# Optimization experiments

Measured on AMD Instinct MI355X. Metric: run time of the kernel, lower is better.

Reference implementation:

```python
import jax, jax.numpy as jnp
import numpy as np

D_IN = 1024
D_OUT = 1024


def setup_inputs() -> dict:
    key = jax.random.key(0)
    kx, kq, kk, kv = jax.random.split(key, 4)
    B, S = 4, 2048
    scale = 1.0 / np.sqrt(D_IN)
    return {
        "x": jax.random.normal(kx, (B, S, D_IN), dtype=jnp.float32),
        "Wq": jax.random.normal(kq, (D_IN, D_OUT), dtype=jnp.float32) * scale,
        "Wk": jax.random.normal(kk, (D_IN, D_OUT), dtype=jnp.float32) * scale,
        "Wv": jax.random.normal(kv, (D_IN, D_OUT), dtype=jnp.float32) * scale,
    }


def reference(x, Wq, Wk, Wv):
    # x: [B, S, D_in]; single-head causal attention (dropout=0 -> identity)
    q = jnp.einsum("bsd,de->bse", x, Wq)
    k = jnp.einsum("bsd,de->bse", x, Wk)
    v = jnp.einsum("bsd,de->bse", x, Wv)
    S = x.shape[1]
    d_k = k.shape[-1]
    scores = jnp.einsum("bqe,bke->bqk", q, k) / jnp.sqrt(jnp.float32(d_k))
    causal = jnp.tril(jnp.ones((S, S), dtype=bool))  # True = keep
    scores = jnp.where(causal, scores, -jnp.inf)
    weights = jax.nn.softmax(scores, axis=-1)
    return jnp.einsum("bqk,bke->bqe", weights, v)
```

## Files before the change

### kernel.cpp

```cpp
#include <hip/hip_runtime.h>

typedef unsigned short u16;
typedef __bf16 bf16x8_v __attribute__((ext_vector_type(8)));
typedef float f32x4 __attribute__((ext_vector_type(4)));

__device__ __forceinline__ u16 f2bf(float f) {
    unsigned u = __float_as_uint(f);
    unsigned r = u + 0x7fffu + ((u >> 16) & 1u);
    return (u16)(r >> 16);
}
__device__ __forceinline__ float bf2f(u16 h) {
    return __uint_as_float(((unsigned)h) << 16);
}

__device__ __forceinline__ void gll16(const u16* g, u16* l) {
    __builtin_amdgcn_global_load_lds(
        (const __attribute__((address_space(1))) void*)g,
        (__attribute__((address_space(3))) void*)l, 16, 0, 0);
}

#define EXP_SHIFT 12.0f

__device__ __forceinline__ float* srow_ptr(u16* Sb, int b, int i) {
    return (float*)((char*)Sb + (size_t)b * 8388608 +
                    ((i >> 9) << 12) + 2048 + ((size_t)(i & 511) << 2));
}

__global__ __launch_bounds__(256) void k_prep(const float* __restrict__ x,
                                              const float* __restrict__ Wq,
                                              const float* __restrict__ Wk,
                                              const float* __restrict__ Wv,
                                              u16* __restrict__ xb,
                                              u16* __restrict__ Wt3,
                                              u16* __restrict__ Sb) {
    __shared__ float tile[32][33];
    const int bid = blockIdx.x, tid = threadIdx.x;
    if (bid < 4096) {
        int i = (bid * 256 + tid) * 8;
        float4 a = *(const float4*)(x + i);
        float4 bb = *(const float4*)(x + i + 4);
        union { int4 p; u16 h[8]; } o;
        o.h[0] = f2bf(a.x);  o.h[1] = f2bf(a.y);  o.h[2] = f2bf(a.z);  o.h[3] = f2bf(a.w);
        o.h[4] = f2bf(bb.x); o.h[5] = f2bf(bb.y); o.h[6] = f2bf(bb.z); o.h[7] = f2bf(bb.w);
        *(int4*)(xb + i) = o.p;
    } else if (bid < 7168) {
        const int w = bid - 4096;
        const int z = w >> 10, rem = w & 1023;
        const int bx = rem & 31, by = rem >> 5;
        const float* W = (z == 0) ? Wq : (z == 1) ? Wk : Wv;
        u16* Wt = Wt3 + (size_t)z * 1024 * 1024;
        const int tx = tid & 31, ty = tid >> 5;
#pragma unroll
        for (int r = 0; r < 4; ++r)
            tile[ty + r * 8][tx] = W[(by * 32 + ty + r * 8) * 1024 + bx * 32 + tx];
        __syncthreads();
#pragma unroll
        for (int r = 0; r < 4; ++r)
            Wt[(bx * 32 + ty + r * 8) * 1024 + by * 32 + tx] =
                f2bf(tile[tx][ty + r * 8]);
    } else {
        const int chunk = tid >> 7;
        const int t = tid & 127;
#pragma unroll
        for (int c = 0; c < 8; ++c) {
            const int cc = c * 2 + chunk;
            char* p = (char*)Sb + (size_t)(cc >> 2) * 8388608 +
                      ((cc & 3) << 12) + 2048;
            int4 z4 = {0, 0, 0, 0};
            *(int4*)(p + t * 16) = z4;
        }
    }
}

__device__ __forceinline__ void gemm_core_nt(const u16* __restrict__ A,
                                             const u16* __restrict__ B,
                                             int lda, int ldb, int kLen,
                                             u16* smem, f32x4 acc[4][4]) {
    u16* As = smem;
    u16* Bs = smem + 128 * 64;
    const int tid = threadIdx.x;
    const int wave = tid >> 6;
    const int lane = tid & 63;
    const int rowA = tid >> 3;
    const int kcs  = (tid & 7) ^ (rowA & 7);
    const int row16 = lane & 15;
    const int quad = lane >> 4;
    const int sw = row16 & 7;
    const int wm = (wave >> 1) * 64;
    const int wn = (wave & 1) * 64;

#pragma unroll
    for (int i = 0; i < 4; ++i)
#pragma unroll
        for (int j = 0; j < 4; ++j) {
            f32x4 z = {0.f, 0.f, 0.f, 0.f};
            acc[i][j] = z;
        }

    const u16* Ag[4]; const u16* Bg[4];
    u16 *AsB[4], *BsB[4];
#pragma unroll
    for (int u = 0; u < 4; ++u) {
        Ag[u] = A + (size_t)(u * 32 + rowA) * lda + kcs * 8;
        Bg[u] = B + (size_t)(u * 32 + rowA) * ldb + kcs * 8;
        AsB[u] = As + (u * 256 + wave * 64) * 8;
        BsB[u] = Bs + (u * 256 + wave * 64) * 8;
    }

    const int ktiles = kLen >> 6;
    for (int kt = 0; kt < ktiles; ++kt) {
        __syncthreads();
#pragma unroll
        for (int u = 0; u < 4; ++u) gll16(Ag[u] + kt * 64, AsB[u]);
#pragma unroll
        for (int u = 0; u < 4; ++u) gll16(Bg[u] + kt * 64, BsB[u]);
        __syncthreads();
#pragma unroll
        for (int h = 0; h < 2; ++h) {
            bf16x8_v af[4], bfv[4];
            const int cp = (h * 4 + quad);
#pragma unroll
            for (int i = 0; i < 4; ++i)
                af[i] = *(const bf16x8_v*)(As + (wm + i * 16 + row16) * 64 +
                                           (cp ^ sw) * 8);
#pragma unroll
            for (int j = 0; j < 4; ++j)
                bfv[j] = *(const bf16x8_v*)(Bs + (wn + j * 16 + row16) * 64 +
                                            (cp ^ sw) * 8);
#pragma unroll
            for (int i = 0; i < 4; ++i)
#pragma unroll
                for (int j = 0; j < 4; ++j)
                    acc[i][j] = __builtin_amdgcn_mfma_f32_16x16x32_bf16(
                        af[i], bfv[j], acc[i][j], 0, 0, 0);
        }
    }
}

__device__ __forceinline__ void epi_bf16(const f32x4 acc[4][4], u16* smem,
                                         u16* __restrict__ g, int ldg) {
    const int tid = threadIdx.x;
    const int wave = tid >> 6, lane = tid & 63;
    const int row16 = lane & 15, quad = lane >> 4;
    u16* Ts = smem + wave * 2048;
#pragma unroll
    for (int jh = 0; jh < 2; ++jh) {
#pragma unroll
        for (int i = 0; i < 4; ++i)
#pragma unroll
            for (int jj = 0; jj < 2; ++jj) {
                const int j = jh * 2 + jj;
#pragma unroll
                for (int r = 0; r < 4; ++r)
                    Ts[(i * 16 + quad * 4 + r) * 32 + jj * 16 + row16] =
                        f2bf(acc[i][j][r]);
            }
#pragma unroll
        for (int s = 0; s < 4; ++s) {
            const int row = s * 16 + (lane >> 2);
            int4 val = *(const int4*)(Ts + row * 32 + (lane & 3) * 8);
            *(int4*)(g + (size_t)row * ldg + jh * 32 + (lane & 3) * 8) = val;
        }
    }
}

__device__ __forceinline__ void epi_vt(const f32x4 acc[4][4], u16* smem,
                                       u16* __restrict__ Vt, int m0w, int n0w) {
    const int tid = threadIdx.x;
    const int wave = tid >> 6, lane = tid & 63;
    const int row16 = lane & 15, quad = lane >> 4;
    const int b = m0w >> 11;
    const int sBase = m0w & 2047;
    u16* Ts = smem + wave * 4608;
#pragma unroll
    for (int p = 0; p < 2; ++p) {
#pragma unroll
        for (int i = 0; i < 4; ++i)
#pragma unroll
            for (int jj = 0; jj < 2; ++jj) {
                const int j = p * 2 + jj;
                union { unsigned long long d; u16 h[4]; } o;
#pragma unroll
                for (int r = 0; r < 4; ++r) o.h[r] = f2bf(acc[i][j][r]);
                *(unsigned long long*)(Ts + (jj * 16 + row16) * 72 +
                                       i * 16 + quad * 4) = o.d;
            }
#pragma unroll
        for (int rr = 0; rr < 4; ++rr) {
            const int ln = rr * 8 + (lane >> 3);
            const int ck = lane & 7;
            int4 val = *(const int4*)(Ts + ln * 72 + ck * 8);
            const int n = n0w + p * 32 + ln;
            *(int4*)(Vt + ((size_t)b * 1024 + n) * 2048 + sBase + ck * 8) = val;
        }
    }
}

__global__ __launch_bounds__(256, 3) void k_gemm_proj(const u16* __restrict__ X,
                                                      const u16* __restrict__ Wt3,
                                                      u16* __restrict__ Qb,
                                                      u16* __restrict__ Kb,
                                                      u16* __restrict__ Vt) {
    __shared__ u16 smem[18432];
    const int n0g = blockIdx.x * 128, m0 = blockIdx.y * 128;
    f32x4 acc[4][4];
    gemm_core_nt(X + (size_t)m0 * 1024, Wt3 + (size_t)n0g * 1024, 1024, 1024, 1024,
                 smem, acc);
    const int tid = threadIdx.x, wave = tid >> 6;
    const int wm = (wave >> 1) * 64, wn = (wave & 1) * 64;
    __syncthreads();
    if (n0g < 2048) {
        u16* Y = (n0g < 1024) ? Qb : Kb;
        const int n0 = n0g & 1023;
        epi_bf16(acc, smem, Y + (size_t)(m0 + wm) * 1024 + n0 + wn, 1024);
    } else {
        epi_vt(acc, smem, Vt, m0 + wm, (n0g - 2048) + wn);
    }
}

__global__ __launch_bounds__(256, 4) void k_gemm_scores(const u16* __restrict__ Q,
                                                        const u16* __restrict__ Kb,
                                                        u16* __restrict__ Sb) {
    __shared__ u16 smem[16384];
    int t = blockIdx.x, b = blockIdx.y;
    int mt = 0;
    while ((mt + 1) * (mt + 2) / 2 <= t) ++mt;
    int nt = t - mt * (mt + 1) / 2;
    const u16* Qp = Q + (size_t)b * 2048 * 1024 + (size_t)mt * 128 * 1024;
    const u16* Kp = Kb + (size_t)b * 2048 * 1024 + (size_t)nt * 128 * 1024;
    u16* Sp = Sb + (size_t)b * 2048 * 2048;
    f32x4 acc[4][4];
    gemm_core_nt(Qp, Kp, 1024, 1024, 1024, smem, acc);
    const int tid = threadIdx.x, wave = tid >> 6, lane = tid & 63;
    const int wm = (wave >> 1) * 64, wn = (wave & 1) * 64;
    const int row16 = lane & 15, quad = lane >> 4;
    const int mBase = mt * 128 + wm;
    const int nBase = nt * 128 + wn;
    u16* Ts = smem + wave * 2048;
    float rs[4][4];
#pragma unroll
    for (int i = 0; i < 4; ++i)
#pragma unroll
        for (int r = 0; r < 4; ++r) rs[i][r] = 0.f;

    __syncthreads();
#pragma unroll
    for (int jh = 0; jh < 2; ++jh) {
#pragma unroll
        for (int i = 0; i < 4; ++i)
#pragma unroll
            for (int jj = 0; jj < 2; ++jj) {
                const int j = jh * 2 + jj;
                const int n = nBase + jh * 32 + jj * 16 + row16;
#pragma unroll
                for (int r = 0; r < 4; ++r) {
                    const int m = mBase + i * 16 + quad * 4 + r;
                    float e = 0.f;
                    if (n <= m)
                        e = __expf(acc[i][j][r] * 0.03125f - EXP_SHIFT);
                    rs[i][r] += e;
                    Ts[(i * 16 + quad * 4 + r) * 32 + jj * 16 + row16] = f2bf(e);
                }
            }
#pragma unroll
        for (int s = 0; s < 4; ++s) {
            const int row = s * 16 + (lane >> 2);
            int4 val = *(const int4*)(Ts + row * 32 + (lane & 3) * 8);
            *(int4*)(Sp + (size_t)(mBase + row) * 2048 +
                     nBase + jh * 32 + (lane & 3) * 8) = val;
        }
    }
#pragma unroll
    for (int i = 0; i < 4; ++i)
#pragma unroll
        for (int r = 0; r < 4; ++r) {
            float s = rs[i][r];
#pragma unroll
            for (int off = 1; off < 16; off <<= 1) s += __shfl_xor(s, off);
            if (row16 == 0)
                atomicAdd(srow_ptr((u16*)Sb, b, mBase + i * 16 + quad * 4 + r), s);
        }
}

__global__ __launch_bounds__(256, 4) void k_gemm_pv(u16* __restrict__ P,
                                                    const u16* __restrict__ Vt,
                                                    float* __restrict__ O) {
    __shared__ u16 smem[16384];
    const int nt = blockIdx.x, mt = 15 - blockIdx.y, b = blockIdx.z;
    const u16* Pp = P + (size_t)b * 2048 * 2048 + (size_t)mt * 128 * 2048;
    const u16* Vp = Vt + (size_t)b * 1024 * 2048 + (size_t)nt * 128 * 2048;
    f32x4 acc[4][4];
    gemm_core_nt(Pp, Vp, 2048, 2048, (mt + 1) * 128, smem, acc);
    float* Op = O + (size_t)b * 2048 * 1024;
    const int tid = threadIdx.x, wave = tid >> 6, lane = tid & 63;
    const int wm = (wave >> 1) * 64, wn = (wave & 1) * 64;
    const int row16 = lane & 15, quad = lane >> 4;
    float inv[4][4];
#pragma unroll
    for (int i = 0; i < 4; ++i)
#pragma unroll
        for (int r = 0; r < 4; ++r)
            inv[i][r] = 1.0f / *srow_ptr(P, b, mt * 128 + wm + i * 16 + quad * 4 + r);
#pragma unroll
    for (int i = 0; i < 4; ++i)
#pragma unroll
        for (int j = 0; j < 4; ++j) {
            int m = mt * 128 + wm + i * 16 + quad * 4;
            int n = nt * 128 + wn + j * 16 + row16;
#pragma unroll
            for (int r = 0; r < 4; ++r)
                Op[(size_t)(m + r) * 1024 + n] = acc[i][j][r] * inv[i][r];
        }
}

extern "C" void kernel_launch(void* const* d_in, const int* in_sizes, int n_in,
                              void* d_out, int out_size, void* d_ws, size_t ws_size,
                              hipStream_t stream) {
    const float* x  = (const float*)d_in[0];
    const float* Wq = (const float*)d_in[1];
    const float* Wk = (const float*)d_in[2];
    const float* Wv = (const float*)d_in[3];
    float* out = (float*)d_out;
    char* ws = (char*)d_ws;

    u16* xb  = (u16*)(ws);
    u16* Wt3 = (u16*)(ws + (16u << 20));
    u16* Qb  = (u16*)(ws + (22u << 20));
    u16* Kb  = (u16*)(ws + (38u << 20));
    u16* Vt  = (u16*)(ws + (54u << 20));
    u16* Sb  = (u16*)(ws + (70u << 20));

    k_prep<<<7169, 256, 0, stream>>>(x, Wq, Wk, Wv, xb, Wt3, Sb);
    k_gemm_proj<<<dim3(24, 64), 256, 0, stream>>>(xb, Wt3, Qb, Kb, Vt);
    k_gemm_scores<<<dim3(136, 4), 256, 0, stream>>>(Qb, Kb, Sb);
    k_gemm_pv<<<dim3(8, 16, 4), 256, 0, stream>>>(Sb, Vt, out);
}
```

Before: 232.0 us.

## Rewrite projection GEMM with 256x256 tiles, 4-stage async LDS pipeline

```diff
diff --git a/kernel.cpp b/kernel.cpp
--- a/kernel.cpp
+++ b/kernel.cpp
@@ -196,25 +196,112 @@
     }
 }
 
-__global__ __launch_bounds__(256, 3) void k_gemm_proj(const u16* __restrict__ X,
-                                                      const u16* __restrict__ Wt3,
-                                                      u16* __restrict__ Qb,
-                                                      u16* __restrict__ Kb,
-                                                      u16* __restrict__ Vt) {
-    __shared__ u16 smem[18432];
-    const int n0g = blockIdx.x * 128, m0 = blockIdx.y * 128;
-    f32x4 acc[4][4];
-    gemm_core_nt(X + (size_t)m0 * 1024, Wt3 + (size_t)n0g * 1024, 1024, 1024, 1024,
-                 smem, acc);
-    const int tid = threadIdx.x, wave = tid >> 6;
-    const int wm = (wave >> 1) * 64, wn = (wave & 1) * 64;
-    __syncthreads();
+__global__ __launch_bounds__(512, 2) void k_gemm_proj2(
+    const u16* __restrict__ X, const u16* __restrict__ Wt3,
+    u16* __restrict__ Qb, u16* __restrict__ Kb, u16* __restrict__ Vt) {
+    extern __shared__ u16 lds[];
+    const int tid = threadIdx.x;
+    const int wave = tid >> 6, lane = tid & 63;
+    const int row16 = lane & 15, quad = lane >> 4;
+
+    const int bid = blockIdx.x;
+    const int lin = (bid & 7) * 48 + (bid >> 3);
+    const int mt = lin / 12, nt = lin - mt * 12;
+    const int m0 = mt << 8, n0g = nt << 8;
+
+    const u16* Ag = X + (size_t)m0 * 1024;
+    const u16* Bg = Wt3 + (size_t)n0g * 1024;
+
+    const int r0 = wave * 32 + (lane >> 2);
+    const int r1 = r0 + 16;
+    const int c0 = (lane & 3) ^ ((r0 >> 1) & 3);
+    const int c1 = (lane & 3) ^ ((r1 >> 1) & 3);
+    const u16* gA0 = Ag + (size_t)r0 * 1024 + c0 * 8;
+    const u16* gA1 = Ag + (size_t)r1 * 1024 + c1 * 8;
+    const u16* gB0 = Bg + (size_t)r0 * 1024 + c0 * 8;
+    const u16* gB1 = Bg + (size_t)r1 * 1024 + c1 * 8;
+    u16* ldsA0 = lds + (wave * 2 + 0) * 512;
+    u16* ldsA1 = lds + (wave * 2 + 1) * 512;
+    u16* ldsB0 = ldsA0 + 8192;
+    u16* ldsB1 = ldsA1 + 8192;
+
+#define STAGE_A(t_) do { const int b_ = ((t_) & 3) * 16384, k_ = (t_) * 32; \
+        gll16(gA0 + k_, ldsA0 + b_); gll16(gA1 + k_, ldsA1 + b_); } while (0)
+#define STAGE_B(t_) do { const int b_ = ((t_) & 3) * 16384, k_ = (t_) * 32; \
+        gll16(gB0 + k_, ldsB0 + b_); gll16(gB1 + k_, ldsB1 + b_); } while (0)
+
+    const int wm = (wave >> 2) * 128, wn = (wave & 3) * 64;
+    const int sw8 = (quad ^ ((row16 >> 1) & 3)) << 3;
+    int offA[8], offB[4];
+#pragma unroll
+    for (int i = 0; i < 8; ++i) offA[i] = (wm + i * 16 + row16) * 32 + sw8;
+#pragma unroll
+    for (int j = 0; j < 4; ++j) offB[j] = (wn + j * 16 + row16) * 32 + sw8 + 8192;
+
+    f32x4 acc[8][4];
+#pragma unroll
+    for (int i = 0; i < 8; ++i)
+#pragma unroll
+        for (int j = 0; j < 4; ++j) { f32x4 z = {0.f, 0.f, 0.f, 0.f}; acc[i][j] = z; }
+
+    const int ktiles = 32;
+    STAGE_A(0); STAGE_B(0);
+    STAGE_A(1); STAGE_B(1);
+    STAGE_A(2); STAGE_B(2);
+
+    for (int t = 0; t < ktiles; ++t) {
+        if (t <= ktiles - 3)
+            asm volatile("s_waitcnt vmcnt(8)" ::: "memory");
+        else if (t == ktiles - 2)
+            asm volatile("s_waitcnt vmcnt(4)" ::: "memory");
+        else
+            asm volatile("s_waitcnt vmcnt(0)" ::: "memory");
+        asm volatile("s_barrier" ::: "memory");
+
+        const u16* buf = lds + (t & 3) * 16384;
+        bf16x8_v bq[4], aq[4];
+#pragma unroll
+        for (int j = 0; j < 4; ++j) bq[j] = *(const bf16x8_v*)(buf + offB[j]);
+#pragma unroll
+        for (int i = 0; i < 4; ++i) aq[i] = *(const bf16x8_v*)(buf + offA[i]);
+        if (t + 3 < ktiles) STAGE_A(t + 3);
+        __builtin_amdgcn_s_setprio(1);
+#pragma unroll
+        for (int i = 0; i < 4; ++i)
+#pragma unroll
+            for (int j = 0; j < 4; ++j)
+                acc[i][j] = __builtin_amdgcn_mfma_f32_16x16x32_bf16(
+                    aq[i], bq[j], acc[i][j], 0, 0, 0);
+        __builtin_amdgcn_s_setprio(0);
+#pragma unroll
+        for (int i = 0; i < 4; ++i) aq[i] = *(const bf16x8_v*)(buf + offA[4 + i]);
+        if (t + 3 < ktiles) STAGE_B(t + 3);
+        __builtin_amdgcn_s_setprio(1);
+#pragma unroll
+        for (int i = 0; i < 4; ++i)
+#pragma unroll
+            for (int j = 0; j < 4; ++j)
+                acc[4 + i][j] = __builtin_amdgcn_mfma_f32_16x16x32_bf16(
+                    aq[i], bq[j], acc[4 + i][j], 0, 0, 0);
+        __builtin_amdgcn_s_setprio(0);
+    }
+#undef STAGE_A
+#undef STAGE_B
+
+    asm volatile("s_waitcnt lgkmcnt(0)" ::: "memory");
+    asm volatile("s_barrier" ::: "memory");
+
     if (n0g < 2048) {
         u16* Y = (n0g < 1024) ? Qb : Kb;
         const int n0 = n0g & 1023;
-        epi_bf16(acc, smem, Y + (size_t)(m0 + wm) * 1024 + n0 + wn, 1024);
+#pragma unroll
+        for (int hf = 0; hf < 2; ++hf)
+            epi_bf16(acc + hf * 4, lds,
+                     Y + (size_t)(m0 + wm + hf * 64) * 1024 + n0 + wn, 1024);
     } else {
-        epi_vt(acc, smem, Vt, m0 + wm, (n0g - 2048) + wn);
+#pragma unroll
+        for (int hf = 0; hf < 2; ++hf)
+            epi_vt(acc + hf * 4, lds, Vt, m0 + wm + hf * 64, (n0g - 2048) + wn);
     }
 }
 
@@ -330,8 +417,15 @@
     u16* Vt  = (u16*)(ws + (54u << 20));
     u16* Sb  = (u16*)(ws + (70u << 20));
 
+    static bool s_attr_done = false;
+    if (!s_attr_done) {
+        hipFuncSetAttribute(reinterpret_cast<const void*>(k_gemm_proj2),
+                            hipFuncAttributeMaxDynamicSharedMemorySize, 131072);
+        s_attr_done = true;
+    }
+
     k_prep<<<7169, 256, 0, stream>>>(x, Wq, Wk, Wv, xb, Wt3, Sb);
-    k_gemm_proj<<<dim3(24, 64), 256, 0, stream>>>(xb, Wt3, Qb, Kb, Vt);
+    k_gemm_proj2<<<dim3(384), dim3(512), 131072, stream>>>(xb, Wt3, Qb, Kb, Vt);
     k_gemm_scores<<<dim3(136, 4), 256, 0, stream>>>(Qb, Kb, Sb);
     k_gemm_pv<<<dim3(8, 16, 4), 256, 0, stream>>>(Sb, Vt, out);
 }
```

After: 236.7 us. 2.0% more time.

## Rewrite QKV projection GEMM as 256x256 ping-pong pipelined kernel with 8 waves

Applied to the files above, without the earlier changes.

```diff
diff --git a/kernel.cpp b/kernel.cpp
--- a/kernel.cpp
+++ b/kernel.cpp
@@ -196,25 +196,134 @@
     }
 }
 
-__global__ __launch_bounds__(256, 3) void k_gemm_proj(const u16* __restrict__ X,
-                                                      const u16* __restrict__ Wt3,
-                                                      u16* __restrict__ Qb,
-                                                      u16* __restrict__ Kb,
-                                                      u16* __restrict__ Vt) {
-    __shared__ u16 smem[18432];
-    const int n0g = blockIdx.x * 128, m0 = blockIdx.y * 128;
-    f32x4 acc[4][4];
-    gemm_core_nt(X + (size_t)m0 * 1024, Wt3 + (size_t)n0g * 1024, 1024, 1024, 1024,
-                 smem, acc);
-    const int tid = threadIdx.x, wave = tid >> 6;
-    const int wm = (wave >> 1) * 64, wn = (wave & 1) * 64;
-    __syncthreads();
+#define BAR  asm volatile("s_barrier" ::: "memory")
+#define VMW4 asm volatile("s_waitcnt vmcnt(4)" ::: "memory")
+#define VMW0 asm volatile("s_waitcnt vmcnt(0)" ::: "memory")
+#define STAGE(LB, GP, KT, H) do { \
+    gll16((GP) + (size_t)((H) * 128) * 1024 + (KT) * 64, \
+          (LB) + ((H) * 128) * 64 + wave * 512); \
+    gll16((GP) + (size_t)((H) * 128 + 64) * 1024 + (KT) * 64, \
+          (LB) + ((H) * 128 + 64) * 64 + wave * 512); } while (0)
+#define LDA_LO(BUF) do { _Pragma("unroll") for (int i = 0; i < 4; ++i) { \
+    a0[i] = *(const bf16x8_v*)((BUF) + offA[i]); \
+    a1[i] = *(const bf16x8_v*)((BUF) + (offA[i] ^ 32)); } } while (0)
+#define LDA_HI(BUF) do { _Pragma("unroll") for (int i = 0; i < 4; ++i) { \
+    a0[i] = *(const bf16x8_v*)((BUF) + offA[4 + i]); \
+    a1[i] = *(const bf16x8_v*)((BUF) + (offA[4 + i] ^ 32)); } } while (0)
+#define LDB_K0(BUF) do { _Pragma("unroll") for (int j = 0; j < 4; ++j) \
+    b0[j] = *(const bf16x8_v*)((BUF) + offB[j]); } while (0)
+#define LDB_K1(BUF) do { _Pragma("unroll") for (int j = 0; j < 4; ++j) \
+    b1[j] = *(const bf16x8_v*)((BUF) + (offB[j] ^ 32)); } while (0)
+#define MFMA16(IOFF, AA, BB) do { __builtin_amdgcn_s_setprio(1); \
+    _Pragma("unroll") for (int i = 0; i < 4; ++i) \
+    _Pragma("unroll") for (int j = 0; j < 4; ++j) \
+        acc[(IOFF) + i][j] = __builtin_amdgcn_mfma_f32_16x16x32_bf16( \
+            AA[i], BB[j], acc[(IOFF) + i][j], 0, 0, 0); \
+    __builtin_amdgcn_s_setprio(0); } while (0)
+
+__global__ __launch_bounds__(512, 2) void k_gemm_proj2(
+    const u16* __restrict__ X, const u16* __restrict__ Wt3,
+    u16* __restrict__ Qb, u16* __restrict__ Kb, u16* __restrict__ Vt) {
+    extern __shared__ u16 lds[];
+    const int tid = threadIdx.x;
+    const int wave = tid >> 6, lane = tid & 63;
+    const int row16 = lane & 15, quad = lane >> 4;
+
+    const int bid = blockIdx.x;
+    const int lin = (bid & 7) * 48 + (bid >> 3);
+    const int mt = lin / 12, nt = lin - mt * 12;
+    const int m0 = mt << 8, n0g = nt << 8;
+
+    const int rowls = wave * 8 + (lane >> 3);
+    const int chk = ((lane & 7) ^ ((lane >> 3) & 7)) << 3;
+    const u16* gA = X + (size_t)(m0 + rowls) * 1024 + chk;
+    const u16* gB = Wt3 + (size_t)(n0g + rowls) * 1024 + chk;
+
+    u16* A0b = lds;
+    u16* B0b = lds + 16384;
+    u16* A1b = lds + 32768;
+    u16* B1b = lds + 49152;
+
+    const int wm = (wave >> 2) * 128, wn = (wave & 3) * 64;
+    const int csw = (quad ^ (row16 & 7)) << 3;
+    int offA[8], offB[4];
+#pragma unroll
+    for (int i = 0; i < 8; ++i) offA[i] = (wm + i * 16 + row16) * 64 + csw;
+#pragma unroll
+    for (int j = 0; j < 4; ++j) offB[j] = (wn + j * 16 + row16) * 64 + csw;
+
+    f32x4 acc[8][4];
+#pragma unroll
+    for (int i = 0; i < 8; ++i)
+#pragma unroll
+        for (int j = 0; j < 4; ++j) { f32x4 z = {0.f, 0.f, 0.f, 0.f}; acc[i][j] = z; }
+
+    STAGE(A0b, gA, 0, 0); STAGE(A0b, gA, 0, 1);
+    STAGE(B0b, gB, 0, 0); STAGE(B0b, gB, 0, 1);
+    STAGE(B1b, gB, 1, 0); STAGE(B1b, gB, 1, 1);
+    VMW4; BAR;
+
+    bf16x8_v a0[4], a1[4], b0[4], b1[4];
+
+    for (int I = 0; I < 7; ++I) {
+        const int kt1 = 2 * I + 1, ktA = 2 * I + 2, ktB = 2 * I + 3;
+        LDA_LO(A0b); LDB_K0(B0b);
+        STAGE(A1b, gA, kt1, 0);
+        BAR; MFMA16(0, a0, b0); BAR;
+        LDB_K1(B0b);
+        STAGE(A1b, gA, kt1, 1);
+        BAR; MFMA16(0, a1, b1); BAR;
+        LDA_HI(A0b);
+        STAGE(B0b, gB, ktA, 0);
+        BAR; MFMA16(4, a0, b0); BAR;
+        STAGE(B0b, gB, ktA, 1);
+        VMW4;
+        BAR; MFMA16(4, a1, b1); BAR;
+        LDA_LO(A1b); LDB_K0(B1b);
+        STAGE(A0b, gA, ktA, 0);
+        BAR; MFMA16(0, a0, b0); BAR;
+        LDB_K1(B1b);
+        STAGE(A0b, gA, ktA, 1);
+        BAR; MFMA16(0, a1, b1); BAR;
+        LDA_HI(A1b);
+        STAGE(B1b, gB, ktB, 0);
+        BAR; MFMA16(4, a0, b0); BAR;
+        STAGE(B1b, gB, ktB, 1);
+        VMW4;
+        BAR; MFMA16(4, a1, b1); BAR;
+    }
+    {
+        LDA_LO(A0b); LDB_K0(B0b);
+        STAGE(A1b, gA, 15, 0);
+        BAR; MFMA16(0, a0, b0); BAR;
+        LDB_K1(B0b);
+        STAGE(A1b, gA, 15, 1);
+        BAR; MFMA16(0, a1, b1); BAR;
+        LDA_HI(A0b);
+        BAR; MFMA16(4, a0, b0); BAR;
+        VMW0;
+        BAR; MFMA16(4, a1, b1); BAR;
+        LDA_LO(A1b); LDB_K0(B1b);
+        BAR; MFMA16(0, a0, b0); BAR;
+        LDB_K1(B1b);
+        BAR; MFMA16(0, a1, b1); BAR;
+        LDA_HI(A1b);
+        BAR; MFMA16(4, a0, b0); BAR;
+        MFMA16(4, a1, b1);
+        BAR;
+    }
+
     if (n0g < 2048) {
         u16* Y = (n0g < 1024) ? Qb : Kb;
         const int n0 = n0g & 1023;
-        epi_bf16(acc, smem, Y + (size_t)(m0 + wm) * 1024 + n0 + wn, 1024);
+#pragma unroll
+        for (int hf = 0; hf < 2; ++hf)
+            epi_bf16(acc + hf * 4, lds,
+                     Y + (size_t)(m0 + wm + hf * 64) * 1024 + n0 + wn, 1024);
     } else {
-        epi_vt(acc, smem, Vt, m0 + wm, (n0g - 2048) + wn);
+#pragma unroll
+        for (int hf = 0; hf < 2; ++hf)
+            epi_vt(acc + hf * 4, lds, Vt, m0 + wm + hf * 64, (n0g - 2048) + wn);
     }
 }
 
@@ -330,8 +439,15 @@
     u16* Vt  = (u16*)(ws + (54u << 20));
     u16* Sb  = (u16*)(ws + (70u << 20));
 
+    static bool s_attr_done = false;
+    if (!s_attr_done) {
+        hipFuncSetAttribute(reinterpret_cast<const void*>(k_gemm_proj2),
+                            hipFuncAttributeMaxDynamicSharedMemorySize, 131072);
+        s_attr_done = true;
+    }
+
     k_prep<<<7169, 256, 0, stream>>>(x, Wq, Wk, Wv, xb, Wt3, Sb);
-    k_gemm_proj<<<dim3(24, 64), 256, 0, stream>>>(xb, Wt3, Qb, Kb, Vt);
+    k_gemm_proj2<<<dim3(384), dim3(512), 131072, stream>>>(xb, Wt3, Qb, Kb, Vt);
     k_gemm_scores<<<dim3(136, 4), 256, 0, stream>>>(Qb, Kb, Sb);
     k_gemm_pv<<<dim3(8, 16, 4), 256, 0, stream>>>(Sb, Vt, out);
 }
```

New measurement: 234.9 us. About the same (+1.3%).

## Fuse scores and PV kernels into persistent kernel with dependency counters

Applied to the files above, without the earlier changes.

```diff
diff --git a/kernel.cpp b/kernel.cpp
--- a/kernel.cpp
+++ b/kernel.cpp
@@ -61,14 +61,16 @@
     } else {
         const int chunk = tid >> 7;
         const int t = tid & 127;
+        int4 z4 = {0, 0, 0, 0};
 #pragma unroll
         for (int c = 0; c < 8; ++c) {
             const int cc = c * 2 + chunk;
             char* p = (char*)Sb + (size_t)(cc >> 2) * 8388608 +
                       ((cc & 3) << 12) + 2048;
-            int4 z4 = {0, 0, 0, 0};
             *(int4*)(p + t * 16) = z4;
         }
+        if (tid < 64)
+            *(int4*)((char*)Sb + 1024 + tid * 16) = z4;
     }
 }
 
@@ -218,99 +220,128 @@
     }
 }
 
-__global__ __launch_bounds__(256, 4) void k_gemm_scores(const u16* __restrict__ Q,
-                                                        const u16* __restrict__ Kb,
-                                                        u16* __restrict__ Sb) {
+__global__ __launch_bounds__(256, 4) void k_sp(const u16* __restrict__ Q,
+                                               const u16* __restrict__ Kb,
+                                               u16* __restrict__ Sb,
+                                               const u16* __restrict__ Vt,
+                                               float* __restrict__ O) {
     __shared__ u16 smem[16384];
-    int t = blockIdx.x, b = blockIdx.y;
-    int mt = 0;
-    while ((mt + 1) * (mt + 2) / 2 <= t) ++mt;
-    int nt = t - mt * (mt + 1) / 2;
-    const u16* Qp = Q + (size_t)b * 2048 * 1024 + (size_t)mt * 128 * 1024;
-    const u16* Kp = Kb + (size_t)b * 2048 * 1024 + (size_t)nt * 128 * 1024;
-    u16* Sp = Sb + (size_t)b * 2048 * 2048;
-    f32x4 acc[4][4];
-    gemm_core_nt(Qp, Kp, 1024, 1024, 1024, smem, acc);
+    __shared__ int s_id;
+    int* ctr = (int*)((char*)Sb + 1024);
     const int tid = threadIdx.x, wave = tid >> 6, lane = tid & 63;
     const int wm = (wave >> 1) * 64, wn = (wave & 1) * 64;
     const int row16 = lane & 15, quad = lane >> 4;
-    const int mBase = mt * 128 + wm;
-    const int nBase = nt * 128 + wn;
-    u16* Ts = smem + wave * 2048;
-    float rs[4][4];
-#pragma unroll
-    for (int i = 0; i < 4; ++i)
-#pragma unroll
-        for (int r = 0; r < 4; ++r) rs[i][r] = 0.f;
-
-    __syncthreads();
-#pragma unroll
-    for (int jh = 0; jh < 2; ++jh) {
-#pragma unroll
-        for (int i = 0; i < 4; ++i)
-#pragma unroll
-            for (int jj = 0; jj < 2; ++jj) {
-                const int j = jh * 2 + jj;
-                const int n = nBase + jh * 32 + jj * 16 + row16;
-#pragma unroll
-                for (int r = 0; r < 4; ++r) {
-                    const int m = mBase + i * 16 + quad * 4 + r;
-                    float e = 0.f;
-                    if (n <= m)
-                        e = __expf(acc[i][j][r] * 0.03125f - EXP_SHIFT);
-                    rs[i][r] += e;
-                    Ts[(i * 16 + quad * 4 + r) * 32 + jj * 16 + row16] = f2bf(e);
+
+    for (;;) {
+        __syncthreads();
+        if (tid == 0)
+            s_id = __hip_atomic_fetch_add(&ctr[0], 1, __ATOMIC_RELAXED,
+                                          __HIP_MEMORY_SCOPE_AGENT);
+        __syncthreads();
+        const int id = s_id;
+        if (id >= 1056) return;
+
+        if (id < 544) {
+            const int b = id / 136;
+            const int t = 135 - (id % 136);
+            int mt = 0;
+            while ((mt + 1) * (mt + 2) / 2 <= t) ++mt;
+            const int nt = t - mt * (mt + 1) / 2;
+            const u16* Qp = Q + (size_t)b * 2048 * 1024 + (size_t)mt * 128 * 1024;
+            const u16* Kp = Kb + (size_t)b * 2048 * 1024 + (size_t)nt * 128 * 1024;
+            u16* Sp = Sb + (size_t)b * 2048 * 2048;
+            f32x4 acc[4][4];
+            gemm_core_nt(Qp, Kp, 1024, 1024, 1024, smem, acc);
+            const int mBase = mt * 128 + wm;
+            const int nBase = nt * 128 + wn;
+            u16* Ts = smem + wave * 2048;
+            float rs[4][4];
+#pragma unroll
+            for (int i = 0; i < 4; ++i)
+#pragma unroll
+                for (int r = 0; r < 4; ++r) rs[i][r] = 0.f;
+
+            __syncthreads();
+#pragma unroll
+            for (int jh = 0; jh < 2; ++jh) {
+#pragma unroll
+                for (int i = 0; i < 4; ++i)
+#pragma unroll
+                    for (int jj = 0; jj < 2; ++jj) {
+                        const int j = jh * 2 + jj;
+                        const int n = nBase + jh * 32 + jj * 16 + row16;
+#pragma unroll
+                        for (int r = 0; r < 4; ++r) {
+                            const int m = mBase + i * 16 + quad * 4 + r;
+                            float e = 0.f;
+                            if (n <= m)
+                                e = __expf(acc[i][j][r] * 0.03125f - EXP_SHIFT);
+                            rs[i][r] += e;
+                            Ts[(i * 16 + quad * 4 + r) * 32 + jj * 16 + row16] =
+                                f2bf(e);
+                        }
+                    }
+#pragma unroll
+                for (int s = 0; s < 4; ++s) {
+                    const int row = s * 16 + (lane >> 2);
+                    int4 val = *(const int4*)(Ts + row * 32 + (lane & 3) * 8);
+                    *(int4*)(Sp + (size_t)(mBase + row) * 2048 +
+                             nBase + jh * 32 + (lane & 3) * 8) = val;
                 }
             }
 #pragma unroll
-        for (int s = 0; s < 4; ++s) {
-            const int row = s * 16 + (lane >> 2);
-            int4 val = *(const int4*)(Ts + row * 32 + (lane & 3) * 8);
-            *(int4*)(Sp + (size_t)(mBase + row) * 2048 +
-                     nBase + jh * 32 + (lane & 3) * 8) = val;
-        }
-    }
-#pragma unroll
-    for (int i = 0; i < 4; ++i)
-#pragma unroll
-        for (int r = 0; r < 4; ++r) {
-            float s = rs[i][r];
-#pragma unroll
-            for (int off = 1; off < 16; off <<= 1) s += __shfl_xor(s, off);
-            if (row16 == 0)
-                atomicAdd(srow_ptr((u16*)Sb, b, mBase + i * 16 + quad * 4 + r), s);
-        }
-}
-
-__global__ __launch_bounds__(256, 4) void k_gemm_pv(u16* __restrict__ P,
-                                                    const u16* __restrict__ Vt,
-                                                    float* __restrict__ O) {
-    __shared__ u16 smem[16384];
-    const int nt = blockIdx.x, mt = 15 - blockIdx.y, b = blockIdx.z;
-    const u16* Pp = P + (size_t)b * 2048 * 2048 + (size_t)mt * 128 * 2048;
-    const u16* Vp = Vt + (size_t)b * 1024 * 2048 + (size_t)nt * 128 * 2048;
-    f32x4 acc[4][4];
-    gemm_core_nt(Pp, Vp, 2048, 2048, (mt + 1) * 128, smem, acc);
-    float* Op = O + (size_t)b * 2048 * 1024;
-    const int tid = threadIdx.x, wave = tid >> 6, lane = tid & 63;
-    const int wm = (wave >> 1) * 64, wn = (wave & 1) * 64;
-    const int row16 = lane & 15, quad = lane >> 4;
-    float inv[4][4];
-#pragma unroll
-    for (int i = 0; i < 4; ++i)
-#pragma unroll
-        for (int r = 0; r < 4; ++r)
-            inv[i][r] = 1.0f / *srow_ptr(P, b, mt * 128 + wm + i * 16 + quad * 4 + r);
-#pragma unroll
-    for (int i = 0; i < 4; ++i)
-#pragma unroll
-        for (int j = 0; j < 4; ++j) {
-            int m = mt * 128 + wm + i * 16 + quad * 4;
-            int n = nt * 128 + wn + j * 16 + row16;
-#pragma unroll
-            for (int r = 0; r < 4; ++r)
-                Op[(size_t)(m + r) * 1024 + n] = acc[i][j][r] * inv[i][r];
-        }
+            for (int i = 0; i < 4; ++i)
+#pragma unroll
+                for (int r = 0; r < 4; ++r) {
+                    float s = rs[i][r];
+#pragma unroll
+                    for (int off = 1; off < 16; off <<= 1) s += __shfl_xor(s, off);
+                    if (row16 == 0)
+                        atomicAdd(srow_ptr(Sb, b, mBase + i * 16 + quad * 4 + r), s);
+                }
+            __threadfence();
+            __syncthreads();
+            if (tid == 0)
+                __hip_atomic_fetch_add(&ctr[2 + b * 16 + mt], 1,
+                                       __ATOMIC_RELEASE,
+                                       __HIP_MEMORY_SCOPE_AGENT);
+        } else {
+            const int p = id - 544;
+            const int mt = 15 - (p >> 5);
+            const int b = (p >> 3) & 3;
+            const int nt = p & 7;
+            if (tid == 0) {
+                while (__hip_atomic_load(&ctr[2 + b * 16 + mt],
+                                         __ATOMIC_RELAXED,
+                                         __HIP_MEMORY_SCOPE_AGENT) < mt + 1)
+                    __builtin_amdgcn_s_sleep(32);
+                __builtin_amdgcn_fence(__ATOMIC_ACQUIRE, "agent");
+            }
+            __syncthreads();
+            const u16* Pp = Sb + (size_t)b * 2048 * 2048 + (size_t)mt * 128 * 2048;
+            const u16* Vp = Vt + (size_t)b * 1024 * 2048 + (size_t)nt * 128 * 2048;
+            f32x4 acc[4][4];
+            gemm_core_nt(Pp, Vp, 2048, 2048, (mt + 1) * 128, smem, acc);
+            float* Op = O + (size_t)b * 2048 * 1024;
+            float inv[4][4];
+#pragma unroll
+            for (int i = 0; i < 4; ++i)
+#pragma unroll
+                for (int r = 0; r < 4; ++r)
+                    inv[i][r] = 1.0f /
+                        *srow_ptr(Sb, b, mt * 128 + wm + i * 16 + quad * 4 + r);
+#pragma unroll
+            for (int i = 0; i < 4; ++i)
+#pragma unroll
+                for (int j = 0; j < 4; ++j) {
+                    int m = mt * 128 + wm + i * 16 + quad * 4;
+                    int n = nt * 128 + wn + j * 16 + row16;
+#pragma unroll
+                    for (int r = 0; r < 4; ++r)
+                        Op[(size_t)(m + r) * 1024 + n] = acc[i][j][r] * inv[i][r];
+                }
+        }
+    }
 }
 
 extern "C" void kernel_launch(void* const* d_in, const int* in_sizes, int n_in,
@@ -332,6 +363,5 @@
 
     k_prep<<<7169, 256, 0, stream>>>(x, Wq, Wk, Wv, xb, Wt3, Sb);
     k_gemm_proj<<<dim3(24, 64), 256, 0, stream>>>(xb, Wt3, Qb, Kb, Vt);
-    k_gemm_scores<<<dim3(136, 4), 256, 0, stream>>>(Qb, Kb, Sb);
-    k_gemm_pv<<<dim3(8, 16, 4), 256, 0, stream>>>(Sb, Vt, out);
-}
+    k_sp<<<1024, 256, 0, stream>>>(Qb, Kb, Sb, Vt, out);
+}
```

Measured after the change: 323.4 us. 39.4% more time.
